# Optimization experiments

Hardware: AMD Instinct MI355X
Metric: run time of the kernel (lower is better)

## Reference

```python
import jax, jax.numpy as jnp
import numpy as np

TEMPERATURE = 0.07
NUM_HARD_NEGATIVES = 5
BATCH, DIM = 4096, 768


def setup_inputs() -> dict:
    key = jax.random.key(0)
    k1, k2 = jax.random.split(key)
    return {
        "text_emb": jax.random.normal(k1, (BATCH, DIM), dtype=jnp.float32),
        "table_emb": jax.random.normal(k2, (BATCH, DIM), dtype=jnp.float32),
    }


def _ttcl_loss(text_emb, table_emb):
    # F.normalize(dim=1)
    t = text_emb / jnp.linalg.norm(text_emb, axis=1, keepdims=True)
    z = table_emb / jnp.linalg.norm(table_emb, axis=1, keepdims=True)
    sim = z @ t.T  # [B, B], sim[i, j] = <table_i, text_j>
    B = sim.shape[0]
    pos = jnp.diagonal(sim) / TEMPERATURE  # [B], <text_i, table_i> == <table_i, text_i>
    diag_mask = jnp.eye(B, dtype=bool)
    neg_inf = jnp.finfo(sim.dtype).min

    def hard_neg_loss(neg_rows):
        # neg_rows[i] holds the B candidate negatives for sample i; exclude self.
        neg = jnp.where(diag_mask, neg_inf, neg_rows)
        top_vals, _ = jax.lax.top_k(neg, NUM_HARD_NEGATIVES)  # [B, k]
        logits = jnp.concatenate([pos[:, None], top_vals / TEMPERATURE], axis=1)  # [B, k+1]
        # cross_entropy with label 0 == -log_softmax(logits)[:, 0]
        return -jax.nn.log_softmax(logits, axis=1)[:, 0]

    # t2z: negatives for i are sim[j][i], j != i  -> column i -> rows of sim.T
    loss_t2z = jnp.sum(hard_neg_loss(sim.T))
    # z2t: negatives for i are sim[i][j], j != i  -> row i
    loss_z2t = jnp.sum(hard_neg_loss(sim))
    loss = (loss_t2z + loss_z2t) / (2 * B)
    return loss, sim


def reference(text_emb, table_emb):
    return _ttcl_loss(text_emb, table_emb)
```

## Files before the change

kernel.cpp:

```cpp
#include <hip/hip_runtime.h>
#include <stdint.h>
#include <math.h>

#define BSZ 4096
#define DIM 768
#define TEMP 0.07f

typedef short short8 __attribute__((ext_vector_type(8)));
typedef float f32x4 __attribute__((ext_vector_type(4)));


__device__ __forceinline__ uint16_t f2bf(float f) {
  uint32_t u = __float_as_uint(f);
  uint32_t r = (u + 0x7FFFu + ((u >> 16) & 1u)) >> 16;
  return (uint16_t)r;
}

__device__ __forceinline__ void gll16(const void* g, void* l) {
  __builtin_amdgcn_global_load_lds(
      (__attribute__((address_space(1))) void*)(uintptr_t)g,
      (__attribute__((address_space(3))) void*)l,
      16, 0, 0);
}

__device__ __forceinline__ void ins5(float v, float& a, float& b, float& c,
                                     float& d, float& e) {
  if (v > e) {
    e = v;
    if (e > d) { float t = d; d = e; e = t;
      if (d > c) { t = c; c = d; d = t;
        if (c > b) { t = b; b = c; c = t;
          if (b > a) { t = a; a = b; b = t; } } } }
  }
}

__device__ __forceinline__ void sins5(float v, float& a, float& b, float& c,
                                      float& d, float& e) {
  float t;
  t = fmaxf(a, v); v = fminf(a, v); a = t;
  t = fmaxf(b, v); v = fminf(b, v); b = t;
  t = fmaxf(c, v); v = fminf(c, v); c = t;
  t = fmaxf(d, v); v = fminf(d, v); d = t;
  e = fmaxf(e, v);
}

__global__ __launch_bounds__(256) void k_norm(const float* __restrict__ text,
                                              const float* __restrict__ table,
                                              uint16_t* __restrict__ tn,
                                              uint16_t* __restrict__ zn) {
  int row = blockIdx.x & (BSZ - 1);
  bool isTable = blockIdx.x >= BSZ;
  const float* src = (isTable ? table : text) + (size_t)row * DIM;
  uint16_t* dst = (isTable ? zn : tn) + (size_t)row * DIM;
  int tid = threadIdx.x;

  float x0 = src[tid];
  float x1 = src[tid + 256];
  float x2 = src[tid + 512];
  float ss = x0 * x0 + x1 * x1 + x2 * x2;
  #pragma unroll
  for (int off = 32; off >= 1; off >>= 1) ss += __shfl_xor(ss, off);
  __shared__ float wss[4];
  if ((tid & 63) == 0) wss[tid >> 6] = ss;
  __syncthreads();
  float inv = rsqrtf(wss[0] + wss[1] + wss[2] + wss[3]);
  dst[tid]       = f2bf(x0 * inv);
  dst[tid + 256] = f2bf(x1 * inv);
  dst[tid + 512] = f2bf(x2 * inv);
}

__global__ __launch_bounds__(512, 2) void k_gemm(const uint16_t* __restrict__ Zb,
                                                 const uint16_t* __restrict__ Tb,
                                                 float* __restrict__ sim) {
  extern __shared__ __attribute__((aligned(16))) char lds[];

  int tid = threadIdx.x;
  int wave = tid >> 6, lane = tid & 63;
  int wm = wave >> 2, wn = wave & 3;
  int brow = (blockIdx.x >> 4) << 8;
  int bcol = (blockIdx.x & 15) << 8;

  f32x4 acc[8][4] = {};

  const uint16_t* gA = Zb + (size_t)brow * DIM + wave * 8;
  const uint16_t* gB = Tb + (size_t)bcol * DIM + wave * 8;
  char* ldsA = lds + (wave << 12);

  int kqg = lane >> 4;
  int rbyte = ((wm << 7) + (lane & 15)) << 4;
  int cbyte = ((wn << 6) + (lane & 15)) << 4;

  auto SA = [&](int t2, int bb, int rg) {
    gll16(gA + (size_t)t2 * 64 + (size_t)(rg * 64 + lane) * DIM,
          ldsA + bb + rg * 1024);
  };
  auto SB = [&](int t2, int bb, int rg) {
    gll16(gB + (size_t)t2 * 64 + (size_t)(rg * 64 + lane) * DIM,
          ldsA + bb + 32768 + rg * 1024);
  };

  auto LOADB = [&](int bb, short8 (&bf)[2][4]) {
    #pragma unroll
    for (int ks = 0; ks < 2; ++ks) {
      const char* Bb = lds + bb + (((ks << 2) + kqg) << 12) + 32768;
      #pragma unroll
      for (int n = 0; n < 4; ++n)
        bf[ks][n] = *(const short8*)(Bb + cbyte + (n << 8));
    }
  };
  auto PHASE = [&](int bb, int mlo, short8 (&bf)[2][4]) {
    __builtin_amdgcn_s_setprio(1);
    #pragma unroll
    for (int ks = 0; ks < 2; ++ks) {
      const char* Ab = lds + bb + (((ks << 2) + kqg) << 12);
      #pragma unroll
      for (int m = 0; m < 4; ++m) {
        short8 af = *(const short8*)(Ab + rbyte + ((mlo + m) << 8));
        #pragma unroll
        for (int n = 0; n < 4; ++n)
          acc[mlo + m][n] = __builtin_amdgcn_mfma_f32_16x16x32_bf16(
              af, bf[ks][n], acc[mlo + m][n], 0, 0, 0);
      }
    }
    __builtin_amdgcn_s_setprio(0);
  };

  #pragma unroll
  for (int rg = 0; rg < 4; ++rg) { SA(0, 0, rg); SB(0, 0, rg); }
  #pragma unroll
  for (int rg = 0; rg < 4; ++rg) { SA(1, 65536, rg); SB(1, 65536, rg); }
  asm volatile("s_waitcnt vmcnt(8)" ::: "memory");
  __builtin_amdgcn_s_barrier();

  #pragma unroll 2
  for (int t = 0; t < 10; ++t) {
    int bb = (t & 1) << 16;
    short8 bf[2][4];
    LOADB(bb, bf);
    PHASE(bb, 0, bf);
    __builtin_amdgcn_s_barrier();
    SA(t + 2, bb, 0); SA(t + 2, bb, 2);
    SB(t + 2, bb, 0); SB(t + 2, bb, 1); SB(t + 2, bb, 2); SB(t + 2, bb, 3);
    PHASE(bb, 4, bf);
    __builtin_amdgcn_s_barrier();
    SA(t + 2, bb, 1); SA(t + 2, bb, 3);
    asm volatile("s_waitcnt vmcnt(8)" ::: "memory");
    __builtin_amdgcn_s_barrier();
  }

  {
    short8 bf[2][4];
    LOADB(0, bf);
    PHASE(0, 0, bf);
    PHASE(0, 4, bf);
  }
  asm volatile("s_waitcnt vmcnt(0)" ::: "memory");
  __builtin_amdgcn_s_barrier();
  {
    short8 bf[2][4];
    LOADB(65536, bf);
    PHASE(65536, 0, bf);
    PHASE(65536, 4, bf);
  }

  int crow0 = brow + (wm << 7) + ((lane >> 4) << 2);
  int ccol0 = bcol + (wn << 6) + (lane & 15);
  #pragma unroll
  for (int m = 0; m < 8; ++m)
    #pragma unroll
    for (int n = 0; n < 4; ++n)
      #pragma unroll
      for (int r = 0; r < 4; ++r)
        sim[(size_t)(crow0 + m * 16 + r) * BSZ + (ccol0 + n * 16)] = acc[m][n][r];
}

__global__ __launch_bounds__(256) void k_tile(const float* __restrict__ sim,
                                              float* __restrict__ rp,
                                              float* __restrict__ cp) {
  extern __shared__ float l32[];
  int tid = threadIdx.x;
  int tr = blockIdx.x >> 5, tc = blockIdx.x & 31;
  int row0 = tr << 7, col0 = tc << 7;
  bool diag = (tr == tc);

  int q = tid & 31;
  int g = tid >> 5;
  const float* gsrc = sim + (size_t)(row0 + (g << 4)) * BSZ + col0 + (q << 2);

  f32x4 v[16];
  #pragma unroll
  for (int k = 0; k < 16; ++k)
    v[k] = *(const f32x4*)(gsrc + (size_t)k * BSZ);

  #pragma unroll
  for (int k = 0; k < 16; ++k) {
    int r = (g << 4) + k;
    if (diag && (r >> 2) == q) v[k][r & 3] = -1e30f;
    *(f32x4*)(l32 + (r << 7) + ((q ^ (r & 7)) << 2)) = v[k];
  }
  __syncthreads();

  {
    int row = tid >> 1, h = tid & 1;
    int rx = row & 7;
    const float* rb = l32 + (row << 7);
    float a0 = -1e30f, a1 = -1e30f, a2 = -1e30f, a3 = -1e30f, a4 = -1e30f;
    #pragma unroll
    for (int j = 0; j < 16; ++j) {
      int c16 = (h << 4) + j;
      f32x4 x = *(const f32x4*)(rb + ((c16 ^ rx) << 2));
      sins5(x[0], a0, a1, a2, a3, a4);
      sins5(x[1], a0, a1, a2, a3, a4);
      sins5(x[2], a0, a1, a2, a3, a4);
      sins5(x[3], a0, a1, a2, a3, a4);
    }
    float b0 = __shfl_xor(a0, 1), b1 = __shfl_xor(a1, 1),
          b2 = __shfl_xor(a2, 1), b3 = __shfl_xor(a3, 1),
          b4 = __shfl_xor(a4, 1);
    sins5(b0, a0, a1, a2, a3, a4);
    sins5(b1, a0, a1, a2, a3, a4);
    sins5(b2, a0, a1, a2, a3, a4);
    sins5(b3, a0, a1, a2, a3, a4);
    sins5(b4, a0, a1, a2, a3, a4);
    if (h == 0) {
      float* pr = rp + ((size_t)(row0 + row) * 32 + tc) * 5;
      pr[0] = a0; pr[1] = a1; pr[2] = a2; pr[3] = a3; pr[4] = a4;
    }
  }

  {
    int c = tid >> 1, hf = tid & 1;
    int cc = c >> 2, cw = c & 3;
    float a0 = -1e30f, a1 = -1e30f, a2 = -1e30f, a3 = -1e30f, a4 = -1e30f;
    #pragma unroll 8
    for (int k = 0; k < 64; ++k) {
      int r = (hf << 6) + k;
      float x = l32[(r << 7) + (((cc ^ (r & 7)) << 2) | cw)];
      sins5(x, a0, a1, a2, a3, a4);
    }
    float b0 = __shfl_xor(a0, 1), b1 = __shfl_xor(a1, 1),
          b2 = __shfl_xor(a2, 1), b3 = __shfl_xor(a3, 1),
          b4 = __shfl_xor(a4, 1);
    sins5(b0, a0, a1, a2, a3, a4);
    sins5(b1, a0, a1, a2, a3, a4);
    sins5(b2, a0, a1, a2, a3, a4);
    sins5(b3, a0, a1, a2, a3, a4);
    sins5(b4, a0, a1, a2, a3, a4);
    if (hf == 0) {
      float* pc = cp + ((size_t)(col0 + c) * 32 + tr) * 5;
      pc[0] = a0; pc[1] = a1; pc[2] = a2; pc[3] = a3; pc[4] = a4;
    }
  }
}

__global__ __launch_bounds__(256) void k_merge(const float* __restrict__ sim,
                                               const float* __restrict__ rp,
                                               const float* __restrict__ cp,
                                               float* __restrict__ lossbuf) {
  int wave = threadIdx.x >> 6, lane = threadIdx.x & 63;
  int wid = blockIdx.x * 4 + wave;
  bool isCol = wid >= BSZ;
  int line = isCol ? wid - BSZ : wid;
  const float* src = (isCol ? cp : rp) + (size_t)line * 160;

  float t0 = -1e30f, t1 = -1e30f, t2 = -1e30f, t3 = -1e30f, t4 = -1e30f;
  ins5(src[lane], t0, t1, t2, t3, t4);
  ins5(src[lane + 64], t0, t1, t2, t3, t4);
  if (lane < 32) ins5(src[lane + 128], t0, t1, t2, t3, t4);

  float top[5];
  #pragma unroll
  for (int e = 0; e < 5; e++) {
    float m = t0;
    #pragma unroll
    for (int off = 32; off >= 1; off >>= 1) m = fmaxf(m, __shfl_xor(m, off));
    unsigned long long msk = __ballot(t0 == m);
    int owner = __ffsll(msk) - 1;
    if (lane == owner) { t0 = t1; t1 = t2; t2 = t3; t3 = t4; t4 = -1e30f; }
    top[e] = m;
  }

  if (lane == 0) {
    float pos = sim[(size_t)line * BSZ + line] / TEMP;
    float l0 = top[0] / TEMP, l1 = top[1] / TEMP, l2 = top[2] / TEMP,
          l3 = top[3] / TEMP, l4 = top[4] / TEMP;
    float mx = fmaxf(pos, fmaxf(fmaxf(l0, l1), fmaxf(fmaxf(l2, l3), l4)));
    float s = expf(pos - mx) + expf(l0 - mx) + expf(l1 - mx) +
              expf(l2 - mx) + expf(l3 - mx) + expf(l4 - mx);
    lossbuf[wid] = mx + logf(s) - pos;
  }
}

__global__ __launch_bounds__(256) void k_reduce(const float* __restrict__ losses,
                                                float* __restrict__ out) {
  int tid = threadIdx.x;
  float s = 0.f;
  for (int i = tid; i < 2 * BSZ; i += 256) s += losses[i];
  #pragma unroll
  for (int off = 32; off >= 1; off >>= 1) s += __shfl_xor(s, off);
  __shared__ float wss[4];
  if ((tid & 63) == 0) wss[tid >> 6] = s;
  __syncthreads();
  if (tid == 0) out[0] = (wss[0] + wss[1] + wss[2] + wss[3]) / (2.0f * BSZ);
}

extern "C" void kernel_launch(void* const* d_in, const int* in_sizes, int n_in,
                              void* d_out, int out_size, void* d_ws, size_t ws_size,
                              hipStream_t stream) {
  const float* text = (const float*)d_in[0];
  const float* table = (const float*)d_in[1];
  float* out = (float*)d_out;
  float* sim = out + 1;

  uint16_t* Zb = (uint16_t*)d_ws;
  uint16_t* Tb = Zb + (size_t)BSZ * DIM;
  float* lossbuf = (float*)(Tb + (size_t)BSZ * DIM);

  float* rp = (float*)d_ws;
  float* cp = rp + (size_t)BSZ * 32 * 5;

  k_norm<<<2 * BSZ, 256, 0, stream>>>(text, table, Tb, Zb);
  k_gemm<<<(BSZ / 256) * (BSZ / 256), 512, 131072, stream>>>(Zb, Tb, sim);
  k_tile<<<32 * 32, 256, 65536, stream>>>(sim, rp, cp);
  k_merge<<<2 * BSZ / 4, 256, 0, stream>>>(sim, rp, cp, lossbuf);
  k_reduce<<<1, 256, 0, stream>>>(lossbuf, out);
}
```

Measured before the change: 89.17 us.

## Switch GEMM LDS tiles to row-major XOR-swizzled layout with coalesced row loads

Global-to-LDS loads now have each group of 8 lanes fetch one full 128-byte row slice, so each wave's global accesses cover contiguous rows instead of striding across 64 rows. The LDS tile becomes row-major with the 16-byte chunk index XOR-swizzled by the row, which is meant to keep MFMA operand reads free of bank conflicts. The A-tile load split across the two half-phases is reorganised by wave group. The risks are extra address arithmetic and a different vmcnt accounting per wave, since waves now issue unequal numbers of loads before the vmcnt(8) wait.

```diff
diff --git a/kernel.cpp b/kernel.cpp
--- a/kernel.cpp
+++ b/kernel.cpp
@@ -82,53 +82,59 @@
 
   f32x4 acc[8][4] = {};
 
-  const uint16_t* gA = Zb + (size_t)brow * DIM + wave * 8;
-  const uint16_t* gB = Tb + (size_t)bcol * DIM + wave * 8;
-  char* ldsA = lds + (wave << 12);
-
+  const uint16_t* gA = Zb + (size_t)brow * DIM;
+  const uint16_t* gB = Tb + (size_t)bcol * DIM;
+
+  int r7 = lane & 7;
   int kqg = lane >> 4;
-  int rbyte = ((wm << 7) + (lane & 15)) << 4;
-  int cbyte = ((wn << 6) + (lane & 15)) << 4;
-
-  auto SA = [&](int t2, int bb, int rg) {
-    gll16(gA + (size_t)t2 * 64 + (size_t)(rg * 64 + lane) * DIM,
-          ldsA + bb + rg * 1024);
+  int rlo = lane & 15;
+
+  int srow = (wave << 5) + (lane >> 3);
+  int sc = ((lane & 7) ^ (srow & 7)) << 3;
+
+  auto SA = [&](int t, int bb, int j) {
+    gll16(gA + (size_t)(srow + j * 8) * DIM + t * 64 + sc,
+          lds + bb + (wave << 12) + (j << 10));
   };
-  auto SB = [&](int t2, int bb, int rg) {
-    gll16(gB + (size_t)t2 * 64 + (size_t)(rg * 64 + lane) * DIM,
-          ldsA + bb + 32768 + rg * 1024);
+  auto SB = [&](int t, int bb, int j) {
+    gll16(gB + (size_t)(srow + j * 8) * DIM + t * 64 + sc,
+          lds + bb + 32768 + (wave << 12) + (j << 10));
   };
 
   auto LOADB = [&](int bb, short8 (&bf)[2][4]) {
+    const char* Bb = lds + bb + 32768;
     #pragma unroll
     for (int ks = 0; ks < 2; ++ks) {
-      const char* Bb = lds + bb + (((ks << 2) + kqg) << 12) + 32768;
+      int ch = (((ks << 2) + kqg) ^ r7) << 4;
       #pragma unroll
-      for (int n = 0; n < 4; ++n)
-        bf[ks][n] = *(const short8*)(Bb + cbyte + (n << 8));
+      for (int n = 0; n < 4; ++n) {
+        int R = (wn << 6) + (n << 4) + rlo;
+        bf[ks][n] = *(const short8*)(Bb + (R << 7) + ch);
+      }
     }
   };
   auto PHASE = [&](int bb, int mlo, short8 (&bf)[2][4]) {
     __builtin_amdgcn_s_setprio(1);
     #pragma unroll
     for (int ks = 0; ks < 2; ++ks) {
-      const char* Ab = lds + bb + (((ks << 2) + kqg) << 12);
+      int ch = (((ks << 2) + kqg) ^ r7) << 4;
       #pragma unroll
-      for (int m = 0; m < 4; ++m) {
-        short8 af = *(const short8*)(Ab + rbyte + ((mlo + m) << 8));
+      for (int mm = 0; mm < 4; ++mm) {
+        int R = (wm << 7) + ((mlo + mm) << 4) + rlo;
+        short8 af = *(const short8*)(lds + bb + (R << 7) + ch);
         #pragma unroll
         for (int n = 0; n < 4; ++n)
-          acc[mlo + m][n] = __builtin_amdgcn_mfma_f32_16x16x32_bf16(
-              af, bf[ks][n], acc[mlo + m][n], 0, 0, 0);
+          acc[mlo + mm][n] = __builtin_amdgcn_mfma_f32_16x16x32_bf16(
+              af, bf[ks][n], acc[mlo + mm][n], 0, 0, 0);
       }
     }
     __builtin_amdgcn_s_setprio(0);
   };
 
   #pragma unroll
-  for (int rg = 0; rg < 4; ++rg) { SA(0, 0, rg); SB(0, 0, rg); }
-  #pragma unroll
-  for (int rg = 0; rg < 4; ++rg) { SA(1, 65536, rg); SB(1, 65536, rg); }
+  for (int j = 0; j < 4; ++j) { SA(0, 0, j); SB(0, 0, j); }
+  #pragma unroll
+  for (int j = 0; j < 4; ++j) { SA(1, 65536, j); SB(1, 65536, j); }
   asm volatile("s_waitcnt vmcnt(8)" ::: "memory");
   __builtin_amdgcn_s_barrier();
 
@@ -139,11 +145,16 @@
     LOADB(bb, bf);
     PHASE(bb, 0, bf);
     __builtin_amdgcn_s_barrier();
-    SA(t + 2, bb, 0); SA(t + 2, bb, 2);
-    SB(t + 2, bb, 0); SB(t + 2, bb, 1); SB(t + 2, bb, 2); SB(t + 2, bb, 3);
+    if ((wave & 2) == 0) {
+      SA(t + 2, bb, 0); SA(t + 2, bb, 1); SA(t + 2, bb, 2); SA(t + 2, bb, 3);
+    }
+    SB(t + 2, bb, 0); SB(t + 2, bb, 1);
+    SB(t + 2, bb, 2); SB(t + 2, bb, 3);
     PHASE(bb, 4, bf);
     __builtin_amdgcn_s_barrier();
-    SA(t + 2, bb, 1); SA(t + 2, bb, 3);
+    if ((wave & 2) != 0) {
+      SA(t + 2, bb, 0); SA(t + 2, bb, 1); SA(t + 2, bb, 2); SA(t + 2, bb, 3);
+    }
     asm volatile("s_waitcnt vmcnt(8)" ::: "memory");
     __builtin_amdgcn_s_barrier();
   }
```

Result: faster. 84.36 us (-5.4%).
